# Kernel optimization log

Measured on AMD Instinct MI355X. Metric: run time of the kernel, lower is better.

## Reference

```python
import jax, jax.numpy as jnp
import numpy as np

EPS = 0.001          # sinkhorn_args['eps']
MAX_ITERS = 100      # sinkhorn_args['max_iters'] (torch early-stops at a fixed point;
                     # running all iters yields the same converged values within tol)


def setup_inputs() -> dict:
    key = jax.random.key(0)
    B, N, d_in, n_ref = 64, 2048, 128, 256
    X = jax.random.normal(key, (B, N, d_in), dtype=jnp.float32)
    # uniform_ref = linspace(-1,1,n_ref) repeated across d_in (the learned parameter's init)
    reference = jnp.tile(jnp.linspace(-1.0, 1.0, n_ref, dtype=jnp.float32)[:, None], (1, d_in))
    return {"X": X, "reference": reference}


def _cdist(a, b):
    # Euclidean pairwise distance (p=2) via gram trick; avoids B x n x m x d blowup.
    a2 = jnp.sum(a * a, axis=-1)[:, :, None]   # (B, n, 1)
    b2 = jnp.sum(b * b, axis=-1)[:, None, :]   # (B, 1, m)
    sq = a2 + b2 - 2.0 * jnp.einsum("bnd,bmd->bnm", a, b)
    return jnp.sqrt(jnp.maximum(sq, 0.0))


def reference(X, reference):
    B, N, d = X.shape
    n_ref = reference.shape[0]
    ref_b = jnp.broadcast_to(reference[None], (B, n_ref, d))
    C = _cdist(ref_b, X)                       # (B, n_ref, N)
    # uniform weights -> scalar log-weights
    log_wx = jnp.log(1.0 / n_ref + 1e-8)
    log_wy = jnp.log(1.0 / N + 1e-8)

    def step(carry, _):
        u, v = carry
        u = EPS * (log_wx - jax.nn.logsumexp((-C + v[:, None, :]) / EPS, axis=2))
        v = EPS * (log_wy - jax.nn.logsumexp((-C + u[:, :, None]) / EPS, axis=1))
        return (u, v), None

    u0 = jnp.zeros((B, n_ref), dtype=C.dtype)
    v0 = jnp.zeros((B, N), dtype=C.dtype)
    (u, v), _ = jax.lax.scan(step, (u0, v0), None, length=MAX_ITERS)

    P = jnp.exp((-C + u[:, :, None] + v[:, None, :]) / EPS)   # transport plan (B, n_ref, N)
    denom = jnp.sum(P, axis=2, keepdims=True) + 1e-8
    barycenters = jnp.einsum("bnm,bmd->bnd", P, X) / denom
    return barycenters - reference[None]       # (B, n_ref, d_in)
```

## Files before the change

kernel.cpp:

```cpp
#include <hip/hip_runtime.h>
#include <math.h>

#define BATCH 64
#define NREF  256
#define NPTS  2048
#define DIM   128
#define ITERS 100
#define C2SCALE 1442.6950408889634f
#define RCH    4
#define NSUB   4
#define NCHUNK 16

#if __has_builtin(__builtin_amdgcn_exp2f)
__device__ __forceinline__ float fexp2(float x) { return __builtin_amdgcn_exp2f(x); }
#else
__device__ __forceinline__ float fexp2(float x) { return exp2f(x); }
#endif
#if __has_builtin(__builtin_amdgcn_logf)
__device__ __forceinline__ float flog2(float x) { return __builtin_amdgcn_logf(x); }
#else
__device__ __forceinline__ float flog2(float x) { return log2f(x); }
#endif


__global__ __launch_bounds__(256) void cgemm_kernel(const float* __restrict__ X,
                                                    const float* __restrict__ ref,
                                                    float* __restrict__ C) {
    __shared__ float rs[8 * 128];
    __shared__ float xs[8 * 128];
    __shared__ float r2s[128];
    __shared__ float x2s[128];
    int b  = blockIdx.x >> 5;
    int it = (blockIdx.x >> 4) & 1;
    int jt = blockIdx.x & 15;
    int i0 = it * 128, j0 = jt * 128;
    int t  = threadIdx.x;
    int ti = t >> 4, tj = t & 15;

    int sr = t >> 1;
    int sh = (t & 1) * 4;
    const float* refp = ref + (size_t)(i0 + sr) * DIM + sh;
    const float* xp   = X + ((size_t)b * NPTS + j0 + sr) * DIM + sh;

    float4 acc[2][2][4];
#pragma unroll
    for (int p = 0; p < 2; ++p)
#pragma unroll
        for (int q = 0; q < 2; ++q)
#pragma unroll
            for (int ii = 0; ii < 4; ++ii)
                acc[p][q][ii] = make_float4(0.f, 0.f, 0.f, 0.f);
    float rsq = 0.f, xsq = 0.f;

    for (int k0 = 0; k0 < DIM; k0 += 8) {
        float4 rv = *(const float4*)(refp + k0);
        float4 xv = *(const float4*)(xp + k0);
        rsq += rv.x * rv.x + rv.y * rv.y + rv.z * rv.z + rv.w * rv.w;
        xsq += xv.x * xv.x + xv.y * xv.y + xv.z * xv.z + xv.w * xv.w;
        __syncthreads();
        rs[(sh + 0) * 128 + sr] = rv.x; rs[(sh + 1) * 128 + sr] = rv.y;
        rs[(sh + 2) * 128 + sr] = rv.z; rs[(sh + 3) * 128 + sr] = rv.w;
        xs[(sh + 0) * 128 + sr] = xv.x; xs[(sh + 1) * 128 + sr] = xv.y;
        xs[(sh + 2) * 128 + sr] = xv.z; xs[(sh + 3) * 128 + sr] = xv.w;
        __syncthreads();

        const float4* rs4 = (const float4*)rs;
        const float4* xs4 = (const float4*)xs;
#pragma unroll
        for (int k = 0; k < 8; ++k) {
            float4 a0 = rs4[k * 32 + ti];
            float4 a1 = rs4[k * 32 + 16 + ti];
            float4 b0 = xs4[k * 32 + tj];
            float4 b1 = xs4[k * 32 + 16 + tj];
#define FMA4(ACC, S, BV)                                                     \
            ACC.x = fmaf(S, BV.x, ACC.x); ACC.y = fmaf(S, BV.y, ACC.y);      \
            ACC.z = fmaf(S, BV.z, ACC.z); ACC.w = fmaf(S, BV.w, ACC.w);
#define ROW(P, S, II)                                                        \
            FMA4(acc[P][0][II], S, b0) FMA4(acc[P][1][II], S, b1)
            ROW(0, a0.x, 0) ROW(0, a0.y, 1) ROW(0, a0.z, 2) ROW(0, a0.w, 3)
            ROW(1, a1.x, 0) ROW(1, a1.y, 1) ROW(1, a1.z, 2) ROW(1, a1.w, 3)
#undef ROW
#undef FMA4
        }
    }

    rsq += __shfl_xor(rsq, 1);
    xsq += __shfl_xor(xsq, 1);
    if ((t & 1) == 0) { r2s[sr] = rsq; x2s[sr] = xsq; }
    __syncthreads();

    float x2v[2][4];
#pragma unroll
    for (int q = 0; q < 2; ++q)
#pragma unroll
        for (int e = 0; e < 4; ++e)
            x2v[q][e] = x2s[q * 64 + tj * 4 + e];

#pragma unroll
    for (int p = 0; p < 2; ++p)
#pragma unroll
        for (int ii = 0; ii < 4; ++ii) {
            int il = p * 64 + ti * 4 + ii;
            float rr = r2s[il];
            float* crow = C + ((size_t)b * NREF + i0 + il) * NPTS + j0;
#pragma unroll
            for (int q = 0; q < 2; ++q) {
                float4 av = acc[p][q][ii];
                float4 o;
                o.x = sqrtf(fmaxf(rr + x2v[q][0] - 2.f * av.x, 0.f)) * C2SCALE;
                o.y = sqrtf(fmaxf(rr + x2v[q][1] - 2.f * av.y, 0.f)) * C2SCALE;
                o.z = sqrtf(fmaxf(rr + x2v[q][2] - 2.f * av.z, 0.f)) * C2SCALE;
                o.w = sqrtf(fmaxf(rr + x2v[q][3] - 2.f * av.w, 0.f)) * C2SCALE;
                *(float4*)(crow + q * 64 + tj * 4) = o;
            }
        }
}

__global__ __launch_bounds__(512, 4) void uv_kernel(const float* __restrict__ C,
                                                    const float* __restrict__ v,
                                                    float* __restrict__ u,
                                                    float* __restrict__ Pl,
                                                    float log_wx) {
    __shared__ float smx[RCH][8];
    __shared__ float sms[RCH][8];
    int b    = blockIdx.x >> 4;
    int co   = blockIdx.x & 15;
    int t    = threadIdx.x;
    int lane = t & 63;
    int w    = t >> 6;

    float4 vj = *(const float4*)(v + (size_t)b * NPTS + 4 * t);
    float4 pm = make_float4(-INFINITY, -INFINITY, -INFINITY, -INFINITY);
    float4 ps = make_float4(0.f, 0.f, 0.f, 0.f);

    for (int cc = 0; cc < NSUB; ++cc) {
        int r0 = co * (RCH * NSUB) + cc * RCH;
        const float* Cb = C + (size_t)(b * NREF + r0) * NPTS;

        float4 a[RCH];
#pragma unroll
        for (int i = 0; i < RCH; ++i)
            a[i] = *(const float4*)(Cb + (size_t)i * NPTS + 4 * t);

        float m[RCH], su[RCH];
#pragma unroll
        for (int i = 0; i < RCH; ++i) {
            a[i].x = vj.x - a[i].x; a[i].y = vj.y - a[i].y;
            a[i].z = vj.z - a[i].z; a[i].w = vj.w - a[i].w;
            m[i] = fmaxf(fmaxf(a[i].x, a[i].y), fmaxf(a[i].z, a[i].w));
        }
#pragma unroll
        for (int i = 0; i < RCH; ++i)
#pragma unroll
            for (int off = 1; off < 64; off <<= 1)
                m[i] = fmaxf(m[i], __shfl_xor(m[i], off));
        if (lane == 0) {
#pragma unroll
            for (int i = 0; i < RCH; ++i) smx[i][w] = m[i];
        }
        __syncthreads();
#pragma unroll
        for (int i = 0; i < RCH; ++i) {
            float mm = smx[i][0];
#pragma unroll
            for (int q = 1; q < 8; ++q) mm = fmaxf(mm, smx[i][q]);
            m[i] = mm;
        }
#pragma unroll
        for (int i = 0; i < RCH; ++i)
            su[i] = fexp2(a[i].x - m[i]) + fexp2(a[i].y - m[i])
                  + fexp2(a[i].z - m[i]) + fexp2(a[i].w - m[i]);
#pragma unroll
        for (int i = 0; i < RCH; ++i)
#pragma unroll
            for (int off = 1; off < 64; off <<= 1)
                su[i] += __shfl_xor(su[i], off);
        if (lane == 0) {
#pragma unroll
            for (int i = 0; i < RCH; ++i) sms[i][w] = su[i];
        }
        __syncthreads();
#pragma unroll
        for (int i = 0; i < RCH; ++i) {
            float s = ((sms[i][0] + sms[i][1]) + (sms[i][2] + sms[i][3]))
                    + ((sms[i][4] + sms[i][5]) + (sms[i][6] + sms[i][7]));
            su[i] = log_wx - (m[i] + flog2(s));
        }
#pragma unroll
        for (int i = 0; i < RCH; ++i)
            if (t == i) u[b * NREF + r0 + i] = su[i];

#pragma unroll
        for (int i = 0; i < RCH; ++i) {
            a[i].x += su[i]; a[i].y += su[i];
            a[i].z += su[i]; a[i].w += su[i];
        }

#define CMERGE(Q)                                                            \
        {                                                                    \
            float mq = a[0].Q;                                               \
            _Pragma("unroll")                                                \
            for (int i_ = 1; i_ < RCH; ++i_)                                 \
                mq = fmaxf(mq, a[i_].Q);                                     \
            float nm = fmaxf(pm.Q, mq);                                      \
            float sq_ = ps.Q * fexp2(pm.Q - nm);                             \
            _Pragma("unroll")                                                \
            for (int i_ = 0; i_ < RCH; ++i_)                                 \
                sq_ += fexp2(a[i_].Q - nm);                                  \
            pm.Q = nm; ps.Q = sq_;                                           \
        }
        CMERGE(x) CMERGE(y) CMERGE(z) CMERGE(w)
#undef CMERGE
    }

    float4 pl;
    pl.x = (pm.x - vj.x) + flog2(ps.x);
    pl.y = (pm.y - vj.y) + flog2(ps.y);
    pl.z = (pm.z - vj.z) + flog2(ps.z);
    pl.w = (pm.w - vj.w) + flog2(ps.w);
    *(float4*)(Pl + (size_t)(b * NCHUNK + co) * NPTS + 4 * t) = pl;
}

__global__ __launch_bounds__(256) void vmerge_kernel(const float* __restrict__ Pl,
                                                     float* __restrict__ v,
                                                     float log_wy) {
    int b = blockIdx.x >> 3;
    int j = ((blockIdx.x & 7) << 8) + threadIdx.x;
    const float* p = Pl + (size_t)b * NCHUNK * NPTS + j;
    float l[NCHUNK];
#pragma unroll
    for (int c = 0; c < NCHUNK; ++c) l[c] = p[(size_t)c * NPTS];
    float m = l[0];
#pragma unroll
    for (int c = 1; c < NCHUNK; ++c) m = fmaxf(m, l[c]);
    float s = 0.f;
#pragma unroll
    for (int c = 0; c < NCHUNK; ++c) s += fexp2(l[c] - m);
    v[(size_t)b * NPTS + j] = log_wy - (m + flog2(s));
}

__global__ __launch_bounds__(512, 2) void out_partialA(const float* __restrict__ C,
                                                       const float* __restrict__ X,
                                                       const float* __restrict__ u,
                                                       const float* __restrict__ v,
                                                       float* __restrict__ Np,
                                                       float* __restrict__ denp) {
    __shared__ float wts[NREF * 16];
    __shared__ float xt[16 * DIM];
    int b  = blockIdx.x >> 3;
    int jc = blockIdx.x & 7;
    int j0 = jc * 256;
    int t  = threadIdx.x;
    int s  = t & 15;
    int g  = t >> 4;

    const float* Cb = C + (size_t)b * NREF * NPTS + j0;
    const float* ub = u + b * NREF;
    const float* vb = v + (size_t)b * NPTS + j0;

    float4 a0[8], a1[8];
    float ws[8];
#pragma unroll
    for (int r = 0; r < 8; ++r) {
        a0[r] = make_float4(0.f, 0.f, 0.f, 0.f);
        a1[r] = make_float4(0.f, 0.f, 0.f, 0.f);
        ws[r] = 0.f;
    }

    for (int jt = 0; jt < 256; jt += 16) {
#pragma unroll
        for (int k = 0; k < 2; ++k) {
            int fidx = t + 512 * k;
            int r = fidx >> 2, q = fidx & 3;
            float4 cv = *(const float4*)(Cb + (size_t)r * NPTS + jt + 4 * q);
            float4 vv = *(const float4*)(vb + jt + 4 * q);
            float uu = ub[r];
            float4 wv;
            wv.x = fexp2(uu + vv.x - cv.x);
            wv.y = fexp2(uu + vv.y - cv.y);
            wv.z = fexp2(uu + vv.z - cv.z);
            wv.w = fexp2(uu + vv.w - cv.w);
            int sw = q ^ ((r >> 3) & 3);
            *(float4*)&wts[r * 16 + sw * 4] = wv;
        }
        const float4* Xb4 = (const float4*)(X + ((size_t)b * NPTS + j0 + jt) * DIM);
        ((float4*)xt)[t] = Xb4[t];
        __syncthreads();

        const float4* xt4 = (const float4*)xt;
#pragma unroll 2
        for (int jp = 0; jp < 8; ++jp) {
            int j1 = 2 * jp;
            float4 xa0 = xt4[j1 * 32 + s];
            float4 xa1 = xt4[j1 * 32 + 16 + s];
            float4 xb0 = xt4[(j1 + 1) * 32 + s];
            float4 xb1 = xt4[(j1 + 1) * 32 + 16 + s];
            int q   = jp >> 1;
            int h   = jp & 1;
            int swb = (q ^ (g & 3)) * 4 + 2 * h;
#pragma unroll
            for (int rr = 0; rr < 8; ++rr) {
                int r = g * 8 + rr;
                float2 w2 = *(const float2*)&wts[r * 16 + swb];
                a0[rr].x = fmaf(w2.x, xa0.x, a0[rr].x);
                a0[rr].y = fmaf(w2.x, xa0.y, a0[rr].y);
                a0[rr].z = fmaf(w2.x, xa0.z, a0[rr].z);
                a0[rr].w = fmaf(w2.x, xa0.w, a0[rr].w);
                a1[rr].x = fmaf(w2.x, xa1.x, a1[rr].x);
                a1[rr].y = fmaf(w2.x, xa1.y, a1[rr].y);
                a1[rr].z = fmaf(w2.x, xa1.z, a1[rr].z);
                a1[rr].w = fmaf(w2.x, xa1.w, a1[rr].w);
                a0[rr].x = fmaf(w2.y, xb0.x, a0[rr].x);
                a0[rr].y = fmaf(w2.y, xb0.y, a0[rr].y);
                a0[rr].z = fmaf(w2.y, xb0.z, a0[rr].z);
                a0[rr].w = fmaf(w2.y, xb0.w, a0[rr].w);
                a1[rr].x = fmaf(w2.y, xb1.x, a1[rr].x);
                a1[rr].y = fmaf(w2.y, xb1.y, a1[rr].y);
                a1[rr].z = fmaf(w2.y, xb1.z, a1[rr].z);
                a1[rr].w = fmaf(w2.y, xb1.w, a1[rr].w);
                ws[rr] += w2.x + w2.y;
            }
        }
        __syncthreads();
    }

    float* npb = Np + ((size_t)jc * BATCH * NREF + (size_t)b * NREF) * DIM;
#pragma unroll
    for (int rr = 0; rr < 8; ++rr) {
        int r = g * 8 + rr;
        float4* nrow = (float4*)(npb + (size_t)r * DIM);
        nrow[s]      = a0[rr];
        nrow[16 + s] = a1[rr];
        if (s == 0) denp[(size_t)jc * BATCH * NREF + b * NREF + r] = ws[rr];
    }
}

__global__ __launch_bounds__(256) void out_finishA(const float* __restrict__ Np,
                                                   const float* __restrict__ denp,
                                                   const float* __restrict__ ref,
                                                   float* __restrict__ out) {
    const int NPL  = BATCH * NREF * DIM / 4;
    const int DENP = BATCH * NREF;
    int fidx = blockIdx.x * 256 + threadIdx.x;
    int bi   = fidx >> 5;
    float4 n4 = make_float4(0.f, 0.f, 0.f, 0.f);
    float dn = 0.f;
    const float4* np4 = (const float4*)Np;
#pragma unroll
    for (int jc = 0; jc < 8; ++jc) {
        float4 p = np4[(size_t)jc * NPL + fidx];
        n4.x += p.x; n4.y += p.y; n4.z += p.z; n4.w += p.w;
        dn += denp[(size_t)jc * DENP + bi];
    }
    float inv = 1.0f / (dn + 1e-8f);
    int i = bi & 255;
    int q = fidx & 31;
    float4 rf = ((const float4*)ref)[i * 32 + q];
    float4 o;
    o.x = n4.x * inv - rf.x;
    o.y = n4.y * inv - rf.y;
    o.z = n4.z * inv - rf.z;
    o.w = n4.w * inv - rf.w;
    ((float4*)out)[fidx] = o;
}

__global__ __launch_bounds__(256) void out_kernelB(const float* __restrict__ C,
                                                   const float* __restrict__ X,
                                                   const float* __restrict__ ref,
                                                   const float* __restrict__ u,
                                                   const float* __restrict__ v,
                                                   float* __restrict__ out) {
    __shared__ float wt[32 * 32];
    __shared__ float xt[32 * DIM];
    int b  = blockIdx.x >> 3;
    int it = blockIdx.x & 7;
    int i0 = it * 32;
    int t  = threadIdx.x;
    int s  = t & 31;
    int g  = t >> 5;

    const float* Cb = C + ((size_t)b * NREF + i0) * NPTS;
    const float* vb = v + (size_t)b * NPTS;
    const float* ub = u + (size_t)b * NREF + i0;

    float4 acc[4];
    float wsum[4];
#pragma unroll
    for (int r = 0; r < 4; ++r) { acc[r] = make_float4(0.f, 0.f, 0.f, 0.f); wsum[r] = 0.f; }

    for (int j0 = 0; j0 < NPTS; j0 += 32) {
#pragma unroll
        for (int k = 0; k < 4; ++k) {
            int widx = t + 256 * k;
            int r    = widx >> 5;
            int jj   = widx & 31;
            wt[widx] = fexp2(ub[r] + vb[j0 + jj] - Cb[(size_t)r * NPTS + j0 + jj]);
        }
        const float4* Xb4 = (const float4*)(X + ((size_t)b * NPTS + j0) * DIM);
#pragma unroll
        for (int k = 0; k < 4; ++k) {
            int idx = t + 256 * k;
            ((float4*)xt)[idx] = Xb4[idx];
        }
        __syncthreads();

        const float4* xt4 = (const float4*)xt;
#pragma unroll 2
        for (int jj = 0; jj < 32; jj += 4) {
            float4 xv0 = xt4[(jj + 0) * 32 + s];
            float4 xv1 = xt4[(jj + 1) * 32 + s];
            float4 xv2 = xt4[(jj + 2) * 32 + s];
            float4 xv3 = xt4[(jj + 3) * 32 + s];
#pragma unroll
            for (int r = 0; r < 4; ++r) {
                float4 w4 = *(const float4*)&wt[(g * 4 + r) * 32 + jj];
                acc[r].x = fmaf(w4.x, xv0.x, acc[r].x); acc[r].y = fmaf(w4.x, xv0.y, acc[r].y);
                acc[r].z = fmaf(w4.x, xv0.z, acc[r].z); acc[r].w = fmaf(w4.x, xv0.w, acc[r].w);
                acc[r].x = fmaf(w4.y, xv1.x, acc[r].x); acc[r].y = fmaf(w4.y, xv1.y, acc[r].y);
                acc[r].z = fmaf(w4.y, xv1.z, acc[r].z); acc[r].w = fmaf(w4.y, xv1.w, acc[r].w);
                acc[r].x = fmaf(w4.z, xv2.x, acc[r].x); acc[r].y = fmaf(w4.z, xv2.y, acc[r].y);
                acc[r].z = fmaf(w4.z, xv2.z, acc[r].z); acc[r].w = fmaf(w4.z, xv2.w, acc[r].w);
                acc[r].x = fmaf(w4.w, xv3.x, acc[r].x); acc[r].y = fmaf(w4.w, xv3.y, acc[r].y);
                acc[r].z = fmaf(w4.w, xv3.z, acc[r].z); acc[r].w = fmaf(w4.w, xv3.w, acc[r].w);
                wsum[r] += (w4.x + w4.y) + (w4.z + w4.w);
            }
        }
        __syncthreads();
    }

#pragma unroll
    for (int r = 0; r < 4; ++r) {
        int i = i0 + g * 4 + r;
        float dn = wsum[r] + 1e-8f;
        float inv = 1.0f / dn;
        float4 rf = ((const float4*)(ref + (size_t)i * DIM))[s];
        float4 o;
        o.x = acc[r].x * inv - rf.x;
        o.y = acc[r].y * inv - rf.y;
        o.z = acc[r].z * inv - rf.z;
        o.w = acc[r].w * inv - rf.w;
        ((float4*)(out + ((size_t)b * NREF + i) * DIM))[s] = o;
    }
}

extern "C" void kernel_launch(void* const* d_in, const int* in_sizes, int n_in,
                              void* d_out, int out_size, void* d_ws, size_t ws_size,
                              hipStream_t stream) {
    const float* X   = (const float*)d_in[0];
    const float* ref = (const float*)d_in[1];
    float* out = (float*)d_out;

    char* ws = (char*)d_ws;
    size_t o = 0;
    float* C = (float*)(ws + o); o += (size_t)BATCH * NREF * NPTS * sizeof(float);
    float* u = (float*)(ws + o); o += (size_t)BATCH * NREF * sizeof(float);
    float* v = (float*)(ws + o); o += (size_t)BATCH * NPTS * sizeof(float);
    float* Pl = (float*)(ws + o);
    float* Np = (float*)(ws + o);
    size_t oA = o + (size_t)8 * BATCH * NREF * DIM * sizeof(float);
    float* denp = (float*)(ws + oA);
    oA += (size_t)8 * BATCH * NREF * sizeof(float);
    bool bigws = (ws_size >= oA);

    const float log_wx = (float)(log(1.0 / (double)NREF + 1e-8) * 1.4426950408889634);
    const float log_wy = (float)(log(1.0 / (double)NPTS + 1e-8) * 1.4426950408889634);

    hipMemsetAsync(v, 0, (size_t)BATCH * NPTS * sizeof(float), stream);

    cgemm_kernel<<<BATCH * 32, 256, 0, stream>>>(X, ref, C);

    for (int t = 0; t < ITERS; ++t) {
        uv_kernel<<<BATCH * NCHUNK, 512, 0, stream>>>(C, v, u, Pl, log_wx);
        vmerge_kernel<<<BATCH * NPTS / 256, 256, 0, stream>>>(Pl, v, log_wy);
    }

    if (bigws) {
        out_partialA<<<BATCH * 8, 512, 0, stream>>>(C, X, u, v, Np, denp);
        out_finishA<<<BATCH * NREF * DIM / 1024, 256, 0, stream>>>(Np, denp, ref, out);
    } else {
        out_kernelB<<<BATCH * 8, 256, 0, stream>>>(C, X, ref, u, v, out);
    }
}
```

Before: 3.632 ms.

## Restructure Sinkhorn uv kernel to one wavefront per 8-row chunk

The u/v update kernel now gives each 64-lane wavefront 8 full rows of C across all 2048 columns. Row max and row sum then reduce with wave shuffles only, removing the shared-memory staging and the block-wide barriers. The per-column online logsumexp uses a single-exp update (lse_step2) instead of a rescale exp plus one exp per element. In exchange, the number of column partial chunks doubles to 32, which raises Pl write traffic and vmerge reads. Fewer and larger thread groups with many live registers may also reduce latency hiding.

```diff
diff --git a/kernel.cpp b/kernel.cpp
--- a/kernel.cpp
+++ b/kernel.cpp
@@ -7,9 +7,8 @@
 #define DIM   128
 #define ITERS 100
 #define C2SCALE 1442.6950408889634f
-#define RCH    4
-#define NSUB   4
-#define NCHUNK 16
+#define RPW    8
+#define NCHUNK 32
 
 #if __has_builtin(__builtin_amdgcn_exp2f)
 __device__ __forceinline__ float fexp2(float x) { return __builtin_amdgcn_exp2f(x); }
@@ -21,6 +20,15 @@
 #else
 __device__ __forceinline__ float flog2(float x) { return log2f(x); }
 #endif
+
+__device__ __forceinline__ void lse_step2(float t, float& m, float& s) {
+    float nm = fmaxf(m, t);
+    float e  = fexp2(m + t - 2.0f * nm);
+    float s1 = fmaf(s, e, 1.0f);
+    float s2 = s + e;
+    s = (t > m) ? s1 : s2;
+    m = nm;
+}
 
 
 __global__ __launch_bounds__(256) void cgemm_kernel(const float* __restrict__ X,
@@ -116,109 +124,75 @@
         }
 }
 
-__global__ __launch_bounds__(512, 4) void uv_kernel(const float* __restrict__ C,
+__global__ __launch_bounds__(256, 2) void uv_kernel(const float* __restrict__ C,
                                                     const float* __restrict__ v,
                                                     float* __restrict__ u,
                                                     float* __restrict__ Pl,
                                                     float log_wx) {
-    __shared__ float smx[RCH][8];
-    __shared__ float sms[RCH][8];
-    int b    = blockIdx.x >> 4;
-    int co   = blockIdx.x & 15;
-    int t    = threadIdx.x;
-    int lane = t & 63;
-    int w    = t >> 6;
-
-    float4 vj = *(const float4*)(v + (size_t)b * NPTS + 4 * t);
-    float4 pm = make_float4(-INFINITY, -INFINITY, -INFINITY, -INFINITY);
-    float4 ps = make_float4(0.f, 0.f, 0.f, 0.f);
-
-    for (int cc = 0; cc < NSUB; ++cc) {
-        int r0 = co * (RCH * NSUB) + cc * RCH;
-        const float* Cb = C + (size_t)(b * NREF + r0) * NPTS;
-
-        float4 a[RCH];
-#pragma unroll
-        for (int i = 0; i < RCH; ++i)
-            a[i] = *(const float4*)(Cb + (size_t)i * NPTS + 4 * t);
-
-        float m[RCH], su[RCH];
-#pragma unroll
-        for (int i = 0; i < RCH; ++i) {
-            a[i].x = vj.x - a[i].x; a[i].y = vj.y - a[i].y;
-            a[i].z = vj.z - a[i].z; a[i].w = vj.w - a[i].w;
-            m[i] = fmaxf(fmaxf(a[i].x, a[i].y), fmaxf(a[i].z, a[i].w));
-        }
-#pragma unroll
-        for (int i = 0; i < RCH; ++i)
-#pragma unroll
-            for (int off = 1; off < 64; off <<= 1)
-                m[i] = fmaxf(m[i], __shfl_xor(m[i], off));
-        if (lane == 0) {
-#pragma unroll
-            for (int i = 0; i < RCH; ++i) smx[i][w] = m[i];
-        }
-        __syncthreads();
-#pragma unroll
-        for (int i = 0; i < RCH; ++i) {
-            float mm = smx[i][0];
-#pragma unroll
-            for (int q = 1; q < 8; ++q) mm = fmaxf(mm, smx[i][q]);
-            m[i] = mm;
-        }
-#pragma unroll
-        for (int i = 0; i < RCH; ++i)
-            su[i] = fexp2(a[i].x - m[i]) + fexp2(a[i].y - m[i])
-                  + fexp2(a[i].z - m[i]) + fexp2(a[i].w - m[i]);
-#pragma unroll
-        for (int i = 0; i < RCH; ++i)
-#pragma unroll
-            for (int off = 1; off < 64; off <<= 1)
-                su[i] += __shfl_xor(su[i], off);
-        if (lane == 0) {
-#pragma unroll
-            for (int i = 0; i < RCH; ++i) sms[i][w] = su[i];
-        }
-        __syncthreads();
-#pragma unroll
-        for (int i = 0; i < RCH; ++i) {
-            float s = ((sms[i][0] + sms[i][1]) + (sms[i][2] + sms[i][3]))
-                    + ((sms[i][4] + sms[i][5]) + (sms[i][6] + sms[i][7]));
-            su[i] = log_wx - (m[i] + flog2(s));
-        }
-#pragma unroll
-        for (int i = 0; i < RCH; ++i)
-            if (t == i) u[b * NREF + r0 + i] = su[i];
-
-#pragma unroll
-        for (int i = 0; i < RCH; ++i) {
-            a[i].x += su[i]; a[i].y += su[i];
-            a[i].z += su[i]; a[i].w += su[i];
-        }
-
-#define CMERGE(Q)                                                            \
-        {                                                                    \
-            float mq = a[0].Q;                                               \
-            _Pragma("unroll")                                                \
-            for (int i_ = 1; i_ < RCH; ++i_)                                 \
-                mq = fmaxf(mq, a[i_].Q);                                     \
-            float nm = fmaxf(pm.Q, mq);                                      \
-            float sq_ = ps.Q * fexp2(pm.Q - nm);                             \
-            _Pragma("unroll")                                                \
-            for (int i_ = 0; i_ < RCH; ++i_)                                 \
-                sq_ += fexp2(a[i_].Q - nm);                                  \
-            pm.Q = nm; ps.Q = sq_;                                           \
-        }
-        CMERGE(x) CMERGE(y) CMERGE(z) CMERGE(w)
-#undef CMERGE
-    }
-
-    float4 pl;
-    pl.x = (pm.x - vj.x) + flog2(ps.x);
-    pl.y = (pm.y - vj.y) + flog2(ps.y);
-    pl.z = (pm.z - vj.z) + flog2(ps.z);
-    pl.w = (pm.w - vj.w) + flog2(ps.w);
-    *(float4*)(Pl + (size_t)(b * NCHUNK + co) * NPTS + 4 * t) = pl;
+    int lane  = threadIdx.x & 63;
+    int gw    = blockIdx.x * 4 + (threadIdx.x >> 6);
+    int b     = gw >> 5;
+    int chunk = gw & 31;
+    const float* Cb = C + (size_t)(b * NREF + chunk * RPW) * NPTS;
+    const float* vb = v + (size_t)b * NPTS;
+    int c0 = 4 * lane;
+
+    float4 pm[8], ps[8];
+#pragma unroll
+    for (int k = 0; k < 8; ++k) {
+        pm[k] = make_float4(-INFINITY, -INFINITY, -INFINITY, -INFINITY);
+        ps[k] = make_float4(0.f, 0.f, 0.f, 0.f);
+    }
+
+#pragma unroll 2
+    for (int r = 0; r < RPW; ++r) {
+        const float* row = Cb + (size_t)r * NPTS;
+        float4 a[8];
+#pragma unroll
+        for (int k = 0; k < 8; ++k) {
+            float4 cv = *(const float4*)(row + k * 256 + c0);
+            float4 vv = *(const float4*)(vb + k * 256 + c0);
+            a[k].x = vv.x - cv.x; a[k].y = vv.y - cv.y;
+            a[k].z = vv.z - cv.z; a[k].w = vv.w - cv.w;
+        }
+        float m = fmaxf(fmaxf(a[0].x, a[0].y), fmaxf(a[0].z, a[0].w));
+#pragma unroll
+        for (int k = 1; k < 8; ++k)
+            m = fmaxf(m, fmaxf(fmaxf(a[k].x, a[k].y), fmaxf(a[k].z, a[k].w)));
+#pragma unroll
+        for (int off = 1; off < 64; off <<= 1)
+            m = fmaxf(m, __shfl_xor(m, off));
+        float s = 0.f;
+#pragma unroll
+        for (int k = 0; k < 8; ++k)
+            s += fexp2(a[k].x - m) + fexp2(a[k].y - m)
+               + fexp2(a[k].z - m) + fexp2(a[k].w - m);
+#pragma unroll
+        for (int off = 1; off < 64; off <<= 1)
+            s += __shfl_xor(s, off);
+        float su = log_wx - (m + flog2(s));
+        if (lane == 0) u[b * NREF + chunk * RPW + r] = su;
+
+#pragma unroll
+        for (int k = 0; k < 8; ++k) {
+            lse_step2(a[k].x + su, pm[k].x, ps[k].x);
+            lse_step2(a[k].y + su, pm[k].y, ps[k].y);
+            lse_step2(a[k].z + su, pm[k].z, ps[k].z);
+            lse_step2(a[k].w + su, pm[k].w, ps[k].w);
+        }
+    }
+
+    float* plb = Pl + (size_t)(b * NCHUNK + chunk) * NPTS;
+#pragma unroll
+    for (int k = 0; k < 8; ++k) {
+        float4 vv = *(const float4*)(vb + k * 256 + c0);
+        float4 pl;
+        pl.x = (pm[k].x - vv.x) + flog2(ps[k].x);
+        pl.y = (pm[k].y - vv.y) + flog2(ps[k].y);
+        pl.z = (pm[k].z - vv.z) + flog2(ps[k].z);
+        pl.w = (pm[k].w - vv.w) + flog2(ps[k].w);
+        *(float4*)(plb + k * 256 + c0) = pl;
+    }
 }
 
 __global__ __launch_bounds__(256) void vmerge_kernel(const float* __restrict__ Pl,
@@ -470,7 +444,7 @@
     cgemm_kernel<<<BATCH * 32, 256, 0, stream>>>(X, ref, C);
 
     for (int t = 0; t < ITERS; ++t) {
-        uv_kernel<<<BATCH * NCHUNK, 512, 0, stream>>>(C, v, u, Pl, log_wx);
+        uv_kernel<<<BATCH * NCHUNK / 4, 256, 0, stream>>>(C, v, u, Pl, log_wx);
         vmerge_kernel<<<BATCH * NPTS / 256, 256, 0, stream>>>(Pl, v, log_wy);
     }
 
```

Measured after the change: 4.216 ms. +16.1%, slower.
